# Kernel optimization log

Measured on AMD Instinct MI355X. Metric: run time of the kernel, lower is better.

## Reference

```python
import jax, jax.numpy as jnp
import numpy as np

B, L, D, H = 1, 4096, 1024, 16
HD = D // H  # head dim = 64
WINDOW = 15


def _rope(t, cos, sin):
    # t: [B,H,L,HD]; cos/sin: [1,1,L,HD//2]
    tr = t.reshape(*t.shape[:-1], HD // 2, 2)
    a, b = tr[..., 0], tr[..., 1]
    out_r = a * cos - b * sin
    out_i = a * sin + b * cos
    return jnp.stack([out_r, out_i], axis=-1).reshape(t.shape)


def _longformer_mask(L, window):
    i = jnp.arange(L)[:, None]
    j = jnp.arange(L)[None, :]
    causal = j <= i
    win = jnp.abs(i - j) <= window // 2
    glob = (j == 0) | (i == 0)
    return (causal & win) | glob  # [L,L] bool


def setup_inputs() -> dict:
    key = jax.random.key(0)
    kx, kq, kk, kv, ko = jax.random.split(key, 5)
    x = jax.random.normal(kx, (B, L, D), dtype=jnp.float32)
    scale = 0.02
    Wq = jax.random.normal(kq, (D, D), dtype=jnp.float32) * scale
    Wk = jax.random.normal(kk, (D, D), dtype=jnp.float32) * scale
    Wv = jax.random.normal(kv, (D, D), dtype=jnp.float32) * scale
    Wo = jax.random.normal(ko, (D, D), dtype=jnp.float32) * scale
    # real RoPE frequencies (complex freqs_cis split into cos/sin)
    inv_freq = 1.0 / (10000.0 ** (np.arange(0, HD, 2, dtype=np.float32) / HD))
    pos = np.arange(L, dtype=np.float32)
    ang = pos[:, None] * inv_freq[None, :]  # [L, HD//2]
    freqs_cos = jnp.asarray(np.cos(ang))[None]  # [1,L,HD//2]
    freqs_sin = jnp.asarray(np.sin(ang))[None]
    return {"x": x, "Wq": Wq, "Wk": Wk, "Wv": Wv, "Wo": Wo,
            "freqs_cos": freqs_cos, "freqs_sin": freqs_sin}


def reference(x, Wq, Wk, Wv, Wo, freqs_cos, freqs_sin):
    b, l, _ = x.shape
    # projections (nn.Linear: y = x @ W^T)
    Q = (x @ Wq.T).reshape(b, l, H, HD).transpose(0, 2, 1, 3)  # [B,H,L,HD]
    K = (x @ Wk.T).reshape(b, l, H, HD).transpose(0, 2, 1, 3)
    V = (x @ Wv.T).reshape(b, l, H, HD).transpose(0, 2, 1, 3)
    cos = freqs_cos[:, None, :l]  # [1,1,L,HD//2] (torch unsqueeze(1))
    sin = freqs_sin[:, None, :l]
    Q = _rope(Q, cos, sin)
    K = _rope(K, cos, sin)
    mask = _longformer_mask(l, WINDOW)  # [L,L]
    scores = jnp.einsum('bhqd,bhkd->bhqk', Q, K) / jnp.sqrt(jnp.float32(HD))
    scores = jnp.where(mask[None, None], scores, jnp.finfo(scores.dtype).min)
    attn = jax.nn.softmax(scores, axis=-1)
    out = jnp.einsum('bhqk,bhkd->bhqd', attn, V)  # [B,H,L,HD]
    out = out.transpose(0, 2, 1, 3).reshape(b, l, D)
    return out @ Wo.T
```

## Files before the change

### kernel.cpp

```cpp
#include <hip/hip_runtime.h>
#include <stdint.h>

#define SL 4096
#define DM 1024
#define NH 16
#define HDIM 64

typedef short short8 __attribute__((ext_vector_type(8)));
typedef float f32x4 __attribute__((ext_vector_type(4)));

__device__ __forceinline__ unsigned short f2bf(float f) {
  unsigned int u = __float_as_uint(f);
  u += 0x7FFF + ((u >> 16) & 1);
  return (unsigned short)(u >> 16);
}
__device__ __forceinline__ float bf2f(unsigned short u) {
  return __uint_as_float((unsigned int)u << 16);
}
__device__ __forceinline__ float bflo(unsigned int u) { return __uint_as_float(u << 16); }
__device__ __forceinline__ float bfhi(unsigned int u) { return __uint_as_float(u & 0xffff0000u); }

__device__ __forceinline__ void gload_lds16(const void* g, void* l) {
  __builtin_amdgcn_global_load_lds((const __attribute__((address_space(1))) void*)g,
                                   (__attribute__((address_space(3))) void*)l, 16, 0, 0);
}
#define SBAR()                                  \
  do {                                          \
    __builtin_amdgcn_sched_barrier(0);          \
    __builtin_amdgcn_s_barrier();               \
    __builtin_amdgcn_sched_barrier(0);          \
  } while (0)
#define LGKM0() asm volatile("s_waitcnt lgkmcnt(0)" ::: "memory")

__global__ void cast_all(const float* __restrict__ x,
                         const float* __restrict__ Wq, const float* __restrict__ Wk,
                         const float* __restrict__ Wv, const float* __restrict__ Wo,
                         unsigned short* __restrict__ xb,
                         unsigned short* __restrict__ w3b, unsigned short* __restrict__ wob) {
  int i = blockIdx.x * blockDim.x + threadIdx.x;
  const float* src;
  unsigned short* dst;
  int off;
  if (i < (1 << 20)) {
    src = x; dst = xb; off = i;
  } else {
    int wsel = i - (1 << 20);
    int seg = wsel >> 18;
    off = wsel & 262143;
    src = (seg == 0) ? Wq : (seg == 1) ? Wk : (seg == 2) ? Wv : Wo;
    dst = (seg < 3) ? (w3b + (size_t)seg * DM * DM) : wob;
  }
  float4 v = ((const float4*)src)[off];
  ushort4 o = make_ushort4(f2bf(v.x), f2bf(v.y), f2bf(v.z), f2bf(v.w));
  ((ushort4*)dst)[off] = o;
}

__global__ __launch_bounds__(512)
void gemm1_rope(const unsigned short* __restrict__ A,
                const unsigned short* __restrict__ B,
                unsigned short* __restrict__ C,
                const float* __restrict__ fc, const float* __restrict__ fs) {
  constexpr int K = 1024, LDA = 1024, LDC = 3072, NT = K / 64;
  __shared__ __align__(16) unsigned short As[2][256 * 64];
  __shared__ __align__(16) unsigned short Bs[2][192 * 64];
  const int tid = threadIdx.x, w = tid >> 6, lane = tid & 63;
  const int wr = w >> 2, wc = w & 3;

  const int gx = gridDim.x;
  const int total = gx * gridDim.y;
  const int lin = blockIdx.y * gx + blockIdx.x;
  const int swz = (lin & 7) * (total >> 3) + (lin >> 3);
  const int brow = (swz / gx) * 256;
  const int bcol = (swz % gx) * 192;

  const unsigned short* gA[2];
  const unsigned short* gB[3];
#pragma unroll
  for (int l = 0; l < 2; ++l) {
    int idx = l * 512 + tid;
    int row_l = idx >> 3, c = idx & 7;
    int csrc = c ^ ((row_l >> 1) & 7);
    gA[l] = A + (size_t)(brow + row_l) * LDA + csrc * 8;
  }
#pragma unroll
  for (int l = 0; l < 3; ++l) {
    int idx = l * 512 + tid;
    int row_l = idx >> 3, c = idx & 7;
    int csrc = c ^ ((row_l >> 1) & 7);
    gB[l] = B + (size_t)(bcol + row_l) * LDA + csrc * 8;
  }

  auto STG_A = [&](int t, int h) {
    const int buf = t & 1;
#pragma unroll
    for (int l = 0; l < 2; ++l)
      gload_lds16(gA[l] + (size_t)h * 128 * LDA + t * 64,
                  &As[buf][h * 8192 + (l * 512 + w * 64) * 8]);
  };
  auto STG_B_a = [&](int t) {
    const int buf = t & 1;
#pragma unroll
    for (int l = 0; l < 2; ++l)
      gload_lds16(gB[l] + t * 64, &Bs[buf][(l * 512 + w * 64) * 8]);
  };
  auto STG_B_b = [&](int t) {
    const int buf = t & 1;
    gload_lds16(gB[2] + t * 64, &Bs[buf][(2 * 512 + w * 64) * 8]);
  };

  const int lrow = lane & 15, h4 = lane >> 4;
  const int g3 = (lane >> 1) & 7;
  const int u2 = h4 ^ (g3 & 3);
  const int gv = g3 >> 2;
  const int co0 = ((((0 ^ gv) << 2) | u2)) * 8;
  const int co1 = ((((1 ^ gv) << 2) | u2)) * 8;

  f32x4 acc[8][3] = {};
  short8 a0[8], a1[8], b0[3], b1[3];

  STG_A(0, 0); STG_A(0, 1); STG_B_a(0); STG_B_b(0); STG_A(1, 0); STG_A(1, 1);
  asm volatile("s_waitcnt vmcnt(4)" ::: "memory");
  SBAR();

  for (int t = 0; t < NT; ++t) {
    const int buf = t & 1;
    const unsigned short* Ab = &As[buf][(wr * 128 + lrow) * 64];
    const unsigned short* Bb = &Bs[buf][(wc * 48 + lrow) * 64];
#pragma unroll
    for (int n = 0; n < 3; ++n) b0[n] = *(const short8*)&Bb[n * 16 * 64 + co0];
#pragma unroll
    for (int m = 0; m < 8; ++m) a0[m] = *(const short8*)&Ab[m * 16 * 64 + co0];
    if (t + 1 < NT) STG_B_a(t + 1);
    SBAR();
    __builtin_amdgcn_s_setprio(1);
#pragma unroll
    for (int m = 0; m < 8; ++m) {
      acc[m][0] = __builtin_amdgcn_mfma_f32_16x16x32_bf16(a0[m], b0[0], acc[m][0], 0, 0, 0);
      acc[m][1] = __builtin_amdgcn_mfma_f32_16x16x32_bf16(a0[m], b0[1], acc[m][1], 0, 0, 0);
    }
    __builtin_amdgcn_s_setprio(0);
#pragma unroll
    for (int n = 0; n < 3; ++n) b1[n] = *(const short8*)&Bb[n * 16 * 64 + co1];
#pragma unroll
    for (int m = 0; m < 8; ++m) a1[m] = *(const short8*)&Ab[m * 16 * 64 + co1];
    if (t + 1 < NT) STG_B_b(t + 1);
    LGKM0();
    SBAR();
    __builtin_amdgcn_s_setprio(1);
#pragma unroll
    for (int m = 0; m < 8; ++m)
      acc[m][2] = __builtin_amdgcn_mfma_f32_16x16x32_bf16(a0[m], b0[2], acc[m][2], 0, 0, 0);
    __builtin_amdgcn_s_setprio(0);
    if (t + 2 < NT) STG_A(t + 2, 0);
    SBAR();
    __builtin_amdgcn_s_setprio(1);
#pragma unroll
    for (int m = 0; m < 8; ++m) {
      acc[m][0] = __builtin_amdgcn_mfma_f32_16x16x32_bf16(a1[m], b1[0], acc[m][0], 0, 0, 0);
      acc[m][1] = __builtin_amdgcn_mfma_f32_16x16x32_bf16(a1[m], b1[1], acc[m][1], 0, 0, 0);
    }
    __builtin_amdgcn_s_setprio(0);
    if (t + 2 < NT) STG_A(t + 2, 1);
    if (t >= NT - 2) {
      asm volatile("s_waitcnt vmcnt(0)" ::: "memory");
    } else {
      asm volatile("s_waitcnt vmcnt(4)" ::: "memory");
    }
    SBAR();
    __builtin_amdgcn_s_setprio(1);
#pragma unroll
    for (int m = 0; m < 8; ++m)
      acc[m][2] = __builtin_amdgcn_mfma_f32_16x16x32_bf16(a1[m], b1[2], acc[m][2], 0, 0, 0);
    __builtin_amdgcn_s_setprio(0);
  }

  const int er = (lane >> 4) * 4;
  const int ec = lane & 15;
#pragma unroll
  for (int n = 0; n < 3; ++n) {
    if (bcol + wc * 48 + n * 16 < 2048) {
      const int p = ((wc * 48 + n * 16 + ec) & 63) >> 1;
#pragma unroll
      for (int m = 0; m < 8; ++m) {
#pragma unroll
        for (int r = 0; r < 4; ++r) {
          const int row = brow + wr * 128 + m * 16 + er + r;
          float v = acc[m][n][r];
          float pv = __shfl_xor(v, 1);
          float cs = fc[row * 32 + p], sn = fs[row * 32 + p];
          acc[m][n][r] = (lane & 1) ? (pv * sn + v * cs) : (v * cs - pv * sn);
        }
      }
    }
  }
#pragma unroll
  for (int m = 0; m < 8; ++m)
#pragma unroll
    for (int n = 0; n < 3; ++n) {
      unsigned short* cp = C + (size_t)(brow + wr * 128 + m * 16 + er) * LDC +
                           (bcol + wc * 48 + n * 16 + ec);
#pragma unroll
      for (int r = 0; r < 4; ++r) cp[(size_t)r * LDC] = f2bf(acc[m][n][r]);
    }
}

__global__ __launch_bounds__(512)
void gemm2_4ph(const unsigned short* __restrict__ A,
               const unsigned short* __restrict__ B,
               float* __restrict__ C) {
  constexpr int K = 1024, LDA = 1024, LDC = 1024, NT = K / 64;
  __shared__ __align__(16) unsigned short As2[2][128 * 64];
  __shared__ __align__(16) unsigned short Bs2[2][128 * 64];
  const int tid = threadIdx.x, w = tid >> 6, lane = tid & 63;
  const int wr = w >> 2, wc = w & 3;

  const int gx = gridDim.x;
  const int total = gx * gridDim.y;
  const int lin = blockIdx.y * gx + blockIdx.x;
  const int swz = (lin & 7) * (total >> 3) + (lin >> 3);
  const int brow = (swz / gx) * 128;
  const int bcol = (swz % gx) * 128;

  const unsigned short* gA[2];
  const unsigned short* gB[2];
#pragma unroll
  for (int l = 0; l < 2; ++l) {
    int idx = l * 512 + tid;
    int row_l = idx >> 3, c = idx & 7;
    int csrc = c ^ ((row_l >> 1) & 7);
    gA[l] = A + (size_t)(brow + row_l) * LDA + csrc * 8;
    gB[l] = B + (size_t)(bcol + row_l) * LDA + csrc * 8;
  }

  auto STG_A = [&](int t, int h) {
    const int buf = t & 1;
    gload_lds16(gA[h] + t * 64, &As2[buf][(h * 512 + w * 64) * 8]);
  };
  auto STG_B = [&](int t, int h) {
    const int buf = t & 1;
    gload_lds16(gB[h] + t * 64, &Bs2[buf][(h * 512 + w * 64) * 8]);
  };

  const int lrow = lane & 15, h4 = lane >> 4;
  const int g3 = (lane >> 1) & 7;
  const int u2 = h4 ^ (g3 & 3);
  const int gv = g3 >> 2;
  const int co0 = ((((0 ^ gv) << 2) | u2)) * 8;
  const int co1 = ((((1 ^ gv) << 2) | u2)) * 8;

  f32x4 acc[4][2] = {};
  short8 a0[4], a1[4], b0[2], b1[2];

  STG_A(0, 0); STG_A(0, 1); STG_B(0, 0); STG_B(0, 1); STG_A(1, 0); STG_A(1, 1);
  asm volatile("s_waitcnt vmcnt(2)" ::: "memory");
  SBAR();

  for (int t = 0; t < NT; ++t) {
    const int buf = t & 1;
    const unsigned short* Ab = &As2[buf][(wr * 64 + lrow) * 64];
    const unsigned short* Bb = &Bs2[buf][(wc * 32 + lrow) * 64];
#pragma unroll
    for (int n = 0; n < 2; ++n) b0[n] = *(const short8*)&Bb[n * 16 * 64 + co0];
#pragma unroll
    for (int m = 0; m < 4; ++m) a0[m] = *(const short8*)&Ab[m * 16 * 64 + co0];
    if (t + 1 < NT) STG_B(t + 1, 0);
    SBAR();
    __builtin_amdgcn_s_setprio(1);
#pragma unroll
    for (int m = 0; m < 4; ++m)
      acc[m][0] = __builtin_amdgcn_mfma_f32_16x16x32_bf16(a0[m], b0[0], acc[m][0], 0, 0, 0);
    __builtin_amdgcn_s_setprio(0);
#pragma unroll
    for (int n = 0; n < 2; ++n) b1[n] = *(const short8*)&Bb[n * 16 * 64 + co1];
#pragma unroll
    for (int m = 0; m < 4; ++m) a1[m] = *(const short8*)&Ab[m * 16 * 64 + co1];
    if (t + 1 < NT) STG_B(t + 1, 1);
    LGKM0();
    SBAR();
    __builtin_amdgcn_s_setprio(1);
#pragma unroll
    for (int m = 0; m < 4; ++m)
      acc[m][1] = __builtin_amdgcn_mfma_f32_16x16x32_bf16(a0[m], b0[1], acc[m][1], 0, 0, 0);
    __builtin_amdgcn_s_setprio(0);
    if (t + 2 < NT) STG_A(t + 2, 0);
    SBAR();
    __builtin_amdgcn_s_setprio(1);
#pragma unroll
    for (int m = 0; m < 4; ++m)
      acc[m][0] = __builtin_amdgcn_mfma_f32_16x16x32_bf16(a1[m], b1[0], acc[m][0], 0, 0, 0);
    __builtin_amdgcn_s_setprio(0);
    if (t + 2 < NT) STG_A(t + 2, 1);
    if (t >= NT - 2) {
      asm volatile("s_waitcnt vmcnt(0)" ::: "memory");
    } else {
      asm volatile("s_waitcnt vmcnt(2)" ::: "memory");
    }
    SBAR();
    __builtin_amdgcn_s_setprio(1);
#pragma unroll
    for (int m = 0; m < 4; ++m)
      acc[m][1] = __builtin_amdgcn_mfma_f32_16x16x32_bf16(a1[m], b1[1], acc[m][1], 0, 0, 0);
    __builtin_amdgcn_s_setprio(0);
  }

  const int er = (lane >> 4) * 4;
  const int ec = lane & 15;
#pragma unroll
  for (int m = 0; m < 4; ++m)
#pragma unroll
    for (int n = 0; n < 2; ++n) {
      float* cp = C + (size_t)(brow + wr * 64 + m * 16 + er) * LDC +
                  (bcol + wc * 32 + n * 16 + ec);
#pragma unroll
      for (int r = 0; r < 4; ++r) cp[(size_t)r * LDC] = acc[m][n][r];
    }
}

__global__ __launch_bounds__(256)
void attn_fused(const unsigned short* __restrict__ qkv, unsigned short* __restrict__ atb,
                float* __restrict__ prt) {
  const int wid = threadIdx.x >> 6;
  const int lane = threadIdx.x & 63;
  if (blockIdx.x >= 1024) {
    const int u = (blockIdx.x - 1024) * 4 + wid;
    const int p = u & 127, h = u >> 7;
    const float q = bf2f(qkv[h * 64 + lane]);
    float m = -1e30f, s = 0.f, o = 0.f;
    const int j0 = p * 32;
    for (int jj = 0; jj < 32; ++jj) {
      const int j = j0 + jj;
      float kv = bf2f(qkv[(size_t)j * 3072 + 1024 + h * 64 + lane]);
      float pr = q * kv;
#pragma unroll
      for (int off = 32; off; off >>= 1) pr += __shfl_xor(pr, off);
      pr *= 0.125f;
      float mn = fmaxf(m, pr);
      float c = __expf(m - mn);
      float e = __expf(pr - mn);
      float v = bf2f(qkv[(size_t)j * 3072 + 2048 + h * 64 + lane]);
      s = s * c + e;
      o = o * c + e * v;
      m = mn;
    }
    float* dst = prt + ((size_t)h * 128 + p) * 72;
    if (lane == 0) { dst[0] = m; dst[1] = s; }
    dst[2 + lane] = o;
    return;
  }

  const int i = blockIdx.x * 4 + wid + 1;
  if (i >= SL) return;
  const unsigned short* rowQ = qkv + (size_t)i * 3072 + lane * 16;

  float q[16];
  {
    uint4 a = *(const uint4*)rowQ;
    uint4 b = *(const uint4*)(rowQ + 8);
    unsigned int uu[8] = {a.x, a.y, a.z, a.w, b.x, b.y, b.z, b.w};
#pragma unroll
    for (int c = 0; c < 8; ++c) { q[2 * c] = bflo(uu[c]); q[2 * c + 1] = bfhi(uu[c]); }
  }

  float sc[9];
#pragma unroll
  for (int t = 0; t < 9; ++t) {
    int j = (t == 0) ? 0 : (i - 8 + t);
    bool valid = (t == 0) || (j >= 1);
    int jc = valid ? j : 0;
    const unsigned short* pk = qkv + (size_t)jc * 3072 + 1024 + lane * 16;
    uint4 a = *(const uint4*)pk;
    uint4 b = *(const uint4*)(pk + 8);
    unsigned int uu[8] = {a.x, a.y, a.z, a.w, b.x, b.y, b.z, b.w};
    float pr = 0.f;
#pragma unroll
    for (int c = 0; c < 8; ++c) pr += bflo(uu[c]) * q[2 * c] + bfhi(uu[c]) * q[2 * c + 1];
    pr += __shfl_xor(pr, 1);
    pr += __shfl_xor(pr, 2);
    sc[t] = valid ? pr * 0.125f : -1e30f;
  }

  float mx = sc[0];
#pragma unroll
  for (int t = 1; t < 9; ++t) mx = fmaxf(mx, sc[t]);
  float s = 0.f;
#pragma unroll
  for (int t = 0; t < 9; ++t) { float e = __expf(sc[t] - mx); sc[t] = e; s += e; }
  const float inv = 1.0f / s;

  float o[16] = {};
#pragma unroll
  for (int t = 0; t < 9; ++t) {
    int j = (t == 0) ? 0 : (i - 8 + t);
    bool valid = (t == 0) || (j >= 1);
    int jc = valid ? j : 0;
    const unsigned short* pv = qkv + (size_t)jc * 3072 + 2048 + lane * 16;
    uint4 a = *(const uint4*)pv;
    uint4 b = *(const uint4*)(pv + 8);
    unsigned int uu[8] = {a.x, a.y, a.z, a.w, b.x, b.y, b.z, b.w};
#pragma unroll
    for (int c = 0; c < 8; ++c) {
      o[2 * c]     += sc[t] * bflo(uu[c]);
      o[2 * c + 1] += sc[t] * bfhi(uu[c]);
    }
  }

  unsigned int wv[8];
#pragma unroll
  for (int c = 0; c < 8; ++c)
    wv[c] = (unsigned int)f2bf(o[2 * c] * inv) | ((unsigned int)f2bf(o[2 * c + 1] * inv) << 16);
  unsigned short* po = atb + (size_t)i * 1024 + lane * 16;
  uint4 s0; s0.x = wv[0]; s0.y = wv[1]; s0.z = wv[2]; s0.w = wv[3];
  uint4 s1; s1.x = wv[4]; s1.y = wv[5]; s1.z = wv[6]; s1.w = wv[7];
  *(uint4*)po = s0;
  *(uint4*)(po + 8) = s1;
}

__global__ __launch_bounds__(64)
void attn_row0_combine(const float* __restrict__ prt, unsigned short* __restrict__ atb) {
  const int h = blockIdx.x;
  const int lane = threadIdx.x;
  const float* base = prt + (size_t)h * 128 * 72;
  __shared__ float cbuf[128];
  float m0 = base[lane * 72];
  float m1 = base[(lane + 64) * 72];
  float M = fmaxf(m0, m1);
#pragma unroll
  for (int off = 32; off; off >>= 1) M = fmaxf(M, __shfl_xor(M, off));
  float c0 = __expf(m0 - M), c1 = __expf(m1 - M);
  float ls = base[lane * 72 + 1] * c0 + base[(lane + 64) * 72 + 1] * c1;
#pragma unroll
  for (int off = 32; off; off >>= 1) ls += __shfl_xor(ls, off);
  cbuf[lane] = c0;
  cbuf[lane + 64] = c1;
  __syncthreads();
  float o = 0.f;
#pragma unroll 8
  for (int p = 0; p < 128; ++p) o += cbuf[p] * base[p * 72 + 2 + lane];
  atb[h * 64 + lane] = f2bf(o / ls);
}

extern "C" void kernel_launch(void* const* d_in, const int* in_sizes, int n_in,
                              void* d_out, int out_size, void* d_ws, size_t ws_size,
                              hipStream_t stream) {
  const float* x  = (const float*)d_in[0];
  const float* Wq = (const float*)d_in[1];
  const float* Wk = (const float*)d_in[2];
  const float* Wv = (const float*)d_in[3];
  const float* Wo = (const float*)d_in[4];
  const float* fc = (const float*)d_in[5];
  const float* fs = (const float*)d_in[6];
  float* out = (float*)d_out;

  char* ws = (char*)d_ws;
  unsigned short* xb   = (unsigned short*)(ws);
  unsigned short* w3b  = (unsigned short*)(ws + ((size_t)8 << 20));
  unsigned short* wob  = (unsigned short*)(ws + ((size_t)14 << 20));
  unsigned short* qkvb = (unsigned short*)(ws + ((size_t)16 << 20));
  unsigned short* atb  = (unsigned short*)(ws + ((size_t)40 << 20));
  float*          prt  = (float*)(ws + ((size_t)48 << 20));

  cast_all<<<(2 * (1 << 20)) / 256, 256, 0, stream>>>(x, Wq, Wk, Wv, Wo, xb, w3b, wob);

  dim3 g1(3072 / 192, SL / 256);
  gemm1_rope<<<g1, 512, 0, stream>>>(xb, w3b, qkvb, fc, fs);

  attn_fused<<<1536, 256, 0, stream>>>(qkvb, atb, prt);
  attn_row0_combine<<<NH, 64, 0, stream>>>(prt, atb);

  dim3 g2(DM / 128, SL / 128);
  gemm2_4ph<<<g2, 512, 0, stream>>>(atb, wob, out);
}
```

Baseline: 90.64 us.

## Prefetch B tiles two stages ahead and fuse row-0 combine via atomic counter

In both GEMM kernels, B-tile global-to-LDS loads are issued two iterations ahead, alongside the A-tile loads, instead of one iteration ahead. The vmcnt waits are widened to match, which gives B loads more time to land before use. Separately, the row-0 global-attention combine is folded into attn_fused with a last-block-done atomic counter per head, removing one kernel launch. The counter is zeroed in cast_all, which adds threadfences and an atomic per partial block.

```diff
diff --git a/kernel.cpp b/kernel.cpp
--- a/kernel.cpp
+++ b/kernel.cpp
@@ -36,8 +36,10 @@
                          const float* __restrict__ Wq, const float* __restrict__ Wk,
                          const float* __restrict__ Wv, const float* __restrict__ Wo,
                          unsigned short* __restrict__ xb,
-                         unsigned short* __restrict__ w3b, unsigned short* __restrict__ wob) {
+                         unsigned short* __restrict__ w3b, unsigned short* __restrict__ wob,
+                         unsigned int* __restrict__ ctr) {
   int i = blockIdx.x * blockDim.x + threadIdx.x;
+  if (i < 16) ctr[i] = 0;
   const float* src;
   unsigned short* dst;
   int off;
@@ -118,8 +120,9 @@
   f32x4 acc[8][3] = {};
   short8 a0[8], a1[8], b0[3], b1[3];
 
-  STG_A(0, 0); STG_A(0, 1); STG_B_a(0); STG_B_b(0); STG_A(1, 0); STG_A(1, 1);
-  asm volatile("s_waitcnt vmcnt(4)" ::: "memory");
+  STG_A(0, 0); STG_A(0, 1); STG_B_a(0); STG_B_b(0);
+  STG_A(1, 0); STG_A(1, 1); STG_B_a(1); STG_B_b(1);
+  asm volatile("s_waitcnt vmcnt(7)" ::: "memory");
   SBAR();
 
   for (int t = 0; t < NT; ++t) {
@@ -130,7 +133,6 @@
     for (int n = 0; n < 3; ++n) b0[n] = *(const short8*)&Bb[n * 16 * 64 + co0];
 #pragma unroll
     for (int m = 0; m < 8; ++m) a0[m] = *(const short8*)&Ab[m * 16 * 64 + co0];
-    if (t + 1 < NT) STG_B_a(t + 1);
     SBAR();
     __builtin_amdgcn_s_setprio(1);
 #pragma unroll
@@ -143,7 +145,6 @@
     for (int n = 0; n < 3; ++n) b1[n] = *(const short8*)&Bb[n * 16 * 64 + co1];
 #pragma unroll
     for (int m = 0; m < 8; ++m) a1[m] = *(const short8*)&Ab[m * 16 * 64 + co1];
-    if (t + 1 < NT) STG_B_b(t + 1);
     LGKM0();
     SBAR();
     __builtin_amdgcn_s_setprio(1);
@@ -151,7 +152,7 @@
     for (int m = 0; m < 8; ++m)
       acc[m][2] = __builtin_amdgcn_mfma_f32_16x16x32_bf16(a0[m], b0[2], acc[m][2], 0, 0, 0);
     __builtin_amdgcn_s_setprio(0);
-    if (t + 2 < NT) STG_A(t + 2, 0);
+    if (t + 2 < NT) { STG_A(t + 2, 0); STG_B_a(t + 2); }
     SBAR();
     __builtin_amdgcn_s_setprio(1);
 #pragma unroll
@@ -160,11 +161,11 @@
       acc[m][1] = __builtin_amdgcn_mfma_f32_16x16x32_bf16(a1[m], b1[1], acc[m][1], 0, 0, 0);
     }
     __builtin_amdgcn_s_setprio(0);
-    if (t + 2 < NT) STG_A(t + 2, 1);
+    if (t + 2 < NT) { STG_A(t + 2, 1); STG_B_b(t + 2); }
     if (t >= NT - 2) {
       asm volatile("s_waitcnt vmcnt(0)" ::: "memory");
     } else {
-      asm volatile("s_waitcnt vmcnt(4)" ::: "memory");
+      asm volatile("s_waitcnt vmcnt(7)" ::: "memory");
     }
     SBAR();
     __builtin_amdgcn_s_setprio(1);
@@ -251,8 +252,9 @@
   f32x4 acc[4][2] = {};
   short8 a0[4], a1[4], b0[2], b1[2];
 
-  STG_A(0, 0); STG_A(0, 1); STG_B(0, 0); STG_B(0, 1); STG_A(1, 0); STG_A(1, 1);
-  asm volatile("s_waitcnt vmcnt(2)" ::: "memory");
+  STG_A(0, 0); STG_A(0, 1); STG_B(0, 0); STG_B(0, 1);
+  STG_A(1, 0); STG_A(1, 1); STG_B(1, 0); STG_B(1, 1);
+  asm volatile("s_waitcnt vmcnt(4)" ::: "memory");
   SBAR();
 
   for (int t = 0; t < NT; ++t) {
@@ -263,7 +265,6 @@
     for (int n = 0; n < 2; ++n) b0[n] = *(const short8*)&Bb[n * 16 * 64 + co0];
 #pragma unroll
     for (int m = 0; m < 4; ++m) a0[m] = *(const short8*)&Ab[m * 16 * 64 + co0];
-    if (t + 1 < NT) STG_B(t + 1, 0);
     SBAR();
     __builtin_amdgcn_s_setprio(1);
 #pragma unroll
@@ -274,7 +275,6 @@
     for (int n = 0; n < 2; ++n) b1[n] = *(const short8*)&Bb[n * 16 * 64 + co1];
 #pragma unroll
     for (int m = 0; m < 4; ++m) a1[m] = *(const short8*)&Ab[m * 16 * 64 + co1];
-    if (t + 1 < NT) STG_B(t + 1, 1);
     LGKM0();
     SBAR();
     __builtin_amdgcn_s_setprio(1);
@@ -282,18 +282,18 @@
     for (int m = 0; m < 4; ++m)
       acc[m][1] = __builtin_amdgcn_mfma_f32_16x16x32_bf16(a0[m], b0[1], acc[m][1], 0, 0, 0);
     __builtin_amdgcn_s_setprio(0);
-    if (t + 2 < NT) STG_A(t + 2, 0);
+    if (t + 2 < NT) { STG_A(t + 2, 0); STG_B(t + 2, 0); }
     SBAR();
     __builtin_amdgcn_s_setprio(1);
 #pragma unroll
     for (int m = 0; m < 4; ++m)
       acc[m][0] = __builtin_amdgcn_mfma_f32_16x16x32_bf16(a1[m], b1[0], acc[m][0], 0, 0, 0);
     __builtin_amdgcn_s_setprio(0);
-    if (t + 2 < NT) STG_A(t + 2, 1);
+    if (t + 2 < NT) { STG_A(t + 2, 1); STG_B(t + 2, 1); }
     if (t >= NT - 2) {
       asm volatile("s_waitcnt vmcnt(0)" ::: "memory");
     } else {
-      asm volatile("s_waitcnt vmcnt(2)" ::: "memory");
+      asm volatile("s_waitcnt vmcnt(4)" ::: "memory");
     }
     SBAR();
     __builtin_amdgcn_s_setprio(1);
@@ -318,7 +318,7 @@
 
 __global__ __launch_bounds__(256)
 void attn_fused(const unsigned short* __restrict__ qkv, unsigned short* __restrict__ atb,
-                float* __restrict__ prt) {
+                float* __restrict__ prt, unsigned int* __restrict__ ctr) {
   const int wid = threadIdx.x >> 6;
   const int lane = threadIdx.x & 63;
   if (blockIdx.x >= 1024) {
@@ -345,6 +345,27 @@
     float* dst = prt + ((size_t)h * 128 + p) * 72;
     if (lane == 0) { dst[0] = m; dst[1] = s; }
     dst[2 + lane] = o;
+    __threadfence();
+    unsigned int old = 0;
+    if (lane == 0) old = atomicAdd(&ctr[h], 1u);
+    old = __shfl(old, 0);
+    if (old == 127u) {
+      __threadfence();
+      const float* base = prt + (size_t)h * 128 * 72;
+      float m0 = base[lane * 72];
+      float m1 = base[(lane + 64) * 72];
+      float M = fmaxf(m0, m1);
+#pragma unroll
+      for (int off = 32; off; off >>= 1) M = fmaxf(M, __shfl_xor(M, off));
+      float ls = 0.f, oo = 0.f;
+#pragma unroll 8
+      for (int pp = 0; pp < 128; ++pp) {
+        float c = __expf(base[pp * 72] - M);
+        ls += c * base[pp * 72 + 1];
+        oo += c * base[pp * 72 + 2 + lane];
+      }
+      atb[h * 64 + lane] = f2bf(oo / ls);
+    }
     return;
   }
 
@@ -413,30 +434,6 @@
   uint4 s1; s1.x = wv[4]; s1.y = wv[5]; s1.z = wv[6]; s1.w = wv[7];
   *(uint4*)po = s0;
   *(uint4*)(po + 8) = s1;
-}
-
-__global__ __launch_bounds__(64)
-void attn_row0_combine(const float* __restrict__ prt, unsigned short* __restrict__ atb) {
-  const int h = blockIdx.x;
-  const int lane = threadIdx.x;
-  const float* base = prt + (size_t)h * 128 * 72;
-  __shared__ float cbuf[128];
-  float m0 = base[lane * 72];
-  float m1 = base[(lane + 64) * 72];
-  float M = fmaxf(m0, m1);
-#pragma unroll
-  for (int off = 32; off; off >>= 1) M = fmaxf(M, __shfl_xor(M, off));
-  float c0 = __expf(m0 - M), c1 = __expf(m1 - M);
-  float ls = base[lane * 72 + 1] * c0 + base[(lane + 64) * 72 + 1] * c1;
-#pragma unroll
-  for (int off = 32; off; off >>= 1) ls += __shfl_xor(ls, off);
-  cbuf[lane] = c0;
-  cbuf[lane + 64] = c1;
-  __syncthreads();
-  float o = 0.f;
-#pragma unroll 8
-  for (int p = 0; p < 128; ++p) o += cbuf[p] * base[p * 72 + 2 + lane];
-  atb[h * 64 + lane] = f2bf(o / ls);
 }
 
 extern "C" void kernel_launch(void* const* d_in, const int* in_sizes, int n_in,
@@ -458,14 +455,14 @@
   unsigned short* qkvb = (unsigned short*)(ws + ((size_t)16 << 20));
   unsigned short* atb  = (unsigned short*)(ws + ((size_t)40 << 20));
   float*          prt  = (float*)(ws + ((size_t)48 << 20));
-
-  cast_all<<<(2 * (1 << 20)) / 256, 256, 0, stream>>>(x, Wq, Wk, Wv, Wo, xb, w3b, wob);
+  unsigned int*   ctr  = (unsigned int*)(ws + ((size_t)49 << 20));
+
+  cast_all<<<(2 * (1 << 20)) / 256, 256, 0, stream>>>(x, Wq, Wk, Wv, Wo, xb, w3b, wob, ctr);
 
   dim3 g1(3072 / 192, SL / 256);
   gemm1_rope<<<g1, 512, 0, stream>>>(xb, w3b, qkvb, fc, fs);
 
-  attn_fused<<<1536, 256, 0, stream>>>(qkvb, atb, prt);
-  attn_row0_combine<<<NH, 64, 0, stream>>>(prt, atb);
+  attn_fused<<<1536, 256, 0, stream>>>(qkvb, atb, prt, ctr);
 
   dim3 g2(DM / 128, SL / 128);
   gemm2_4ph<<<g2, 512, 0, stream>>>(atb, wob, out);
```

Result: slower. 162.7 us (+79.5%).
